# Performance work log

Measured on AMD Instinct MI355X. Metric: run time of the kernel, lower is better.

## Reference

```python
import jax, jax.numpy as jnp
import numpy as np

MARGIN = 1.0

def setup_inputs() -> dict:
    key = jax.random.key(0)
    B = 8192
    sim = jax.random.normal(key, (B, B), dtype=jnp.float32)
    return {"sim": sim}

def _half_loss(mat, offdiag):
    # mat: [B, B]; per-row pos = diagonal, neg = max over off-diag entries
    # satisfying neg + margin > pos. Rows with no valid neg are skipped (0).
    pos = jnp.diagonal(mat)                                   # [B]
    valid = offdiag & (mat + MARGIN > pos[:, None])           # [B, B]
    neg = jnp.max(jnp.where(valid, mat, -jnp.inf), axis=1)    # [B]
    has = jnp.any(valid, axis=1)                              # [B]
    neg_safe = jnp.where(has, neg, 0.0)
    pos_loss = jnp.clip(0.2 * pos * pos - 0.7 * pos + 0.5, 0.0)
    neg_loss = jnp.clip(0.9 * neg_safe * neg_safe - 0.4 * neg_safe + 0.03, 0.0)
    return jnp.sum(jnp.where(has, pos_loss + neg_loss, 0.0))

def reference(sim):
    B = sim.shape[0]
    offdiag = ~jnp.eye(B, dtype=bool)
    total = _half_loss(sim, offdiag) + _half_loss(sim.T, offdiag)
    return total / B
```

## Files before the change

### kernel.cpp

```cpp
#include <hip/hip_runtime.h>
#include <math.h>
#include <limits.h>

#define BN 8192
#define ROWS 32
#define TPB 256
#define NCB 8

__device__ __forceinline__ int map_f(float x) {
    int b = __float_as_int(x);
    return b >= 0 ? b : b ^ 0x7fffffff;
}
__device__ __forceinline__ float unmap_f(int m) {
    int b = m >= 0 ? m : m ^ 0x7fffffff;
    return __int_as_float(b);
}

__global__ __launch_bounds__(1024) void init_kernel(int* __restrict__ maxes) {
    int i = blockIdx.x * blockDim.x + threadIdx.x;
    if (i < 2 * BN) maxes[i] = INT_MIN;
}

__global__ __launch_bounds__(TPB) void max_kernel(const float* __restrict__ sim,
                                                  int* __restrict__ row_max_i,
                                                  int* __restrict__ col_max_i,
                                                  float* __restrict__ diag) {
    __shared__ float lds[ROWS * 4];
    const int t = threadIdx.x;
    const int bid = blockIdx.x;
    const int cb = bid & (NCB - 1);
    const int rbase = (bid >> 3) * ROWS;
    const int gf = cb * TPB + t;

    float4 cm = make_float4(-INFINITY, -INFINITY, -INFINITY, -INFINITY);

#pragma unroll 4
    for (int r = 0; r < ROWS; ++r) {
        const int gr = rbase + r;
        float4 v = ((const float4*)(sim + (size_t)gr * BN))[gf];
        if (gf == (gr >> 2)) {
            diag[gr] = ((float*)&v)[gr & 3];
            ((float*)&v)[gr & 3] = -INFINITY;
        }
        cm.x = fmaxf(cm.x, v.x);
        cm.y = fmaxf(cm.y, v.y);
        cm.z = fmaxf(cm.z, v.z);
        cm.w = fmaxf(cm.w, v.w);
        float m = fmaxf(fmaxf(v.x, v.y), fmaxf(v.z, v.w));
#pragma unroll
        for (int off = 32; off > 0; off >>= 1)
            m = fmaxf(m, __shfl_down(m, off, 64));
        if ((t & 63) == 0) lds[r * 4 + (t >> 6)] = m;
    }
    __syncthreads();
    if (t < ROWS) {
        float m = fmaxf(fmaxf(lds[t * 4 + 0], lds[t * 4 + 1]),
                        fmaxf(lds[t * 4 + 2], lds[t * 4 + 3]));
        atomicMax(&row_max_i[rbase + t], map_f(m));
    }
    const int c = 4 * gf;
    atomicMax(&col_max_i[c + 0], map_f(cm.x));
    atomicMax(&col_max_i[c + 1], map_f(cm.y));
    atomicMax(&col_max_i[c + 2], map_f(cm.z));
    atomicMax(&col_max_i[c + 3], map_f(cm.w));
}

__global__ __launch_bounds__(1024) void loss_kernel(const float* __restrict__ diag,
                                                    const int* __restrict__ row_max_i,
                                                    const int* __restrict__ col_max_i,
                                                    float* __restrict__ out) {
    __shared__ float lds[16];
    const int t = threadIdx.x;
    float sum = 0.0f;
#pragma unroll
    for (int k = 0; k < BN / 1024; ++k) {
        const int i = t + 1024 * k;
        const float pos = diag[i];
        const float pos_loss = fmaxf(0.2f * pos * pos - 0.7f * pos + 0.5f, 0.0f);

        const float rneg = unmap_f(row_max_i[i]);
        if (rneg + 1.0f > pos)
            sum += pos_loss + fmaxf(0.9f * rneg * rneg - 0.4f * rneg + 0.03f, 0.0f);

        const float cneg = unmap_f(col_max_i[i]);
        if (cneg + 1.0f > pos)
            sum += pos_loss + fmaxf(0.9f * cneg * cneg - 0.4f * cneg + 0.03f, 0.0f);
    }
#pragma unroll
    for (int off = 32; off > 0; off >>= 1)
        sum += __shfl_down(sum, off, 64);
    if ((t & 63) == 0) lds[t >> 6] = sum;
    __syncthreads();
    if (t == 0) {
        float total = 0.0f;
        for (int w = 0; w < 16; ++w) total += lds[w];
        out[0] = total / (float)BN;
    }
}

extern "C" void kernel_launch(void* const* d_in, const int* in_sizes, int n_in,
                              void* d_out, int out_size, void* d_ws, size_t ws_size,
                              hipStream_t stream) {
    const float* sim = (const float*)d_in[0];
    int*   row_max_i = (int*)d_ws;
    int*   col_max_i = (int*)((char*)d_ws + BN * sizeof(int));
    float* diag      = (float*)((char*)d_ws + 2 * BN * sizeof(int));
    float* out = (float*)d_out;

    init_kernel<<<(2 * BN) / 1024, 1024, 0, stream>>>(row_max_i);
    max_kernel<<<(BN / ROWS) * NCB, TPB, 0, stream>>>(sim, row_max_i, col_max_i, diag);
    loss_kernel<<<1, 1024, 0, stream>>>(diag, row_max_i, col_max_i, out);
}
```

Measured before the change: 377.4 us.

## Replace global atomic max reductions with partial buffers and a two-stage reduce

The max kernel now writes per-block row and column partial maxima to workspace buffers instead of issuing global atomicMax on integer-mapped floats. This also removes the init kernel. A new 64-block reduce kernel combines the partials and computes per-block loss sums, and a tiny final kernel sums those. This swaps atomic contention on 8192 column addresses for an extra 8 MB write and read of column partials.

```diff
diff --git a/kernel.cpp b/kernel.cpp
--- a/kernel.cpp
+++ b/kernel.cpp
@@ -1,35 +1,23 @@
 #include <hip/hip_runtime.h>
 #include <math.h>
-#include <limits.h>
 
 #define BN 8192
 #define ROWS 32
 #define TPB 256
 #define NCB 8
-
-__device__ __forceinline__ int map_f(float x) {
-    int b = __float_as_int(x);
-    return b >= 0 ? b : b ^ 0x7fffffff;
-}
-__device__ __forceinline__ float unmap_f(int m) {
-    int b = m >= 0 ? m : m ^ 0x7fffffff;
-    return __int_as_float(b);
-}
-
-__global__ __launch_bounds__(1024) void init_kernel(int* __restrict__ maxes) {
-    int i = blockIdx.x * blockDim.x + threadIdx.x;
-    if (i < 2 * BN) maxes[i] = INT_MIN;
-}
+#define NRG 256
+#define RBLK 64
 
 __global__ __launch_bounds__(TPB) void max_kernel(const float* __restrict__ sim,
-                                                  int* __restrict__ row_max_i,
-                                                  int* __restrict__ col_max_i,
+                                                  float* __restrict__ rowpart,
+                                                  float* __restrict__ colpart,
                                                   float* __restrict__ diag) {
     __shared__ float lds[ROWS * 4];
     const int t = threadIdx.x;
     const int bid = blockIdx.x;
     const int cb = bid & (NCB - 1);
-    const int rbase = (bid >> 3) * ROWS;
+    const int rg = bid >> 3;
+    const int rbase = rg * ROWS;
     const int gf = cb * TPB + t;
 
     float4 cm = make_float4(-INFINITY, -INFINITY, -INFINITY, -INFINITY);
@@ -56,58 +44,79 @@
     if (t < ROWS) {
         float m = fmaxf(fmaxf(lds[t * 4 + 0], lds[t * 4 + 1]),
                         fmaxf(lds[t * 4 + 2], lds[t * 4 + 3]));
-        atomicMax(&row_max_i[rbase + t], map_f(m));
+        rowpart[cb * BN + rbase + t] = m;
     }
-    const int c = 4 * gf;
-    atomicMax(&col_max_i[c + 0], map_f(cm.x));
-    atomicMax(&col_max_i[c + 1], map_f(cm.y));
-    atomicMax(&col_max_i[c + 2], map_f(cm.z));
-    atomicMax(&col_max_i[c + 3], map_f(cm.w));
+    ((float4*)(colpart + (size_t)rg * BN))[gf] = cm;
 }
 
-__global__ __launch_bounds__(1024) void loss_kernel(const float* __restrict__ diag,
-                                                    const int* __restrict__ row_max_i,
-                                                    const int* __restrict__ col_max_i,
-                                                    float* __restrict__ out) {
-    __shared__ float lds[16];
+__global__ __launch_bounds__(TPB) void reduce_loss(const float* __restrict__ rowpart,
+                                                   const float* __restrict__ colpart,
+                                                   const float* __restrict__ diag,
+                                                   float* __restrict__ block_sums) {
+    __shared__ float csh[TPB];
+    __shared__ float psum[4];
     const int t = threadIdx.x;
+    const int blk = blockIdx.x;
+    const int c = blk * 128 + (t & 127);
+    const int h = t >> 7;
+
+    float c0 = -INFINITY, c1 = -INFINITY, c2 = -INFINITY, c3 = -INFINITY;
+    for (int j = 0; j < 128; j += 4) {
+        const size_t base = (size_t)(h * 128 + j) * BN + c;
+        c0 = fmaxf(c0, colpart[base]);
+        c1 = fmaxf(c1, colpart[base + (size_t)BN]);
+        c2 = fmaxf(c2, colpart[base + (size_t)2 * BN]);
+        c3 = fmaxf(c3, colpart[base + (size_t)3 * BN]);
+    }
+    csh[t] = fmaxf(fmaxf(c0, c1), fmaxf(c2, c3));
+    __syncthreads();
+
     float sum = 0.0f;
+    if (t < 128) {
+        const int i = blk * 128 + t;
+        const float cneg = fmaxf(csh[t], csh[t + 128]);
+        float rneg = -INFINITY;
 #pragma unroll
-    for (int k = 0; k < BN / 1024; ++k) {
-        const int i = t + 1024 * k;
+        for (int cb = 0; cb < NCB; ++cb)
+            rneg = fmaxf(rneg, rowpart[cb * BN + i]);
         const float pos = diag[i];
         const float pos_loss = fmaxf(0.2f * pos * pos - 0.7f * pos + 0.5f, 0.0f);
-
-        const float rneg = unmap_f(row_max_i[i]);
         if (rneg + 1.0f > pos)
             sum += pos_loss + fmaxf(0.9f * rneg * rneg - 0.4f * rneg + 0.03f, 0.0f);
-
-        const float cneg = unmap_f(col_max_i[i]);
         if (cneg + 1.0f > pos)
             sum += pos_loss + fmaxf(0.9f * cneg * cneg - 0.4f * cneg + 0.03f, 0.0f);
     }
 #pragma unroll
     for (int off = 32; off > 0; off >>= 1)
         sum += __shfl_down(sum, off, 64);
-    if ((t & 63) == 0) lds[t >> 6] = sum;
+    if ((t & 63) == 0) psum[t >> 6] = sum;
     __syncthreads();
-    if (t == 0) {
-        float total = 0.0f;
-        for (int w = 0; w < 16; ++w) total += lds[w];
-        out[0] = total / (float)BN;
-    }
+    if (t == 0)
+        block_sums[blk] = (psum[0] + psum[1]) + (psum[2] + psum[3]);
+}
+
+__global__ __launch_bounds__(64) void final_kernel(const float* __restrict__ block_sums,
+                                                   float* __restrict__ out) {
+    const int t = threadIdx.x;
+    float s = block_sums[t];
+#pragma unroll
+    for (int off = 32; off > 0; off >>= 1)
+        s += __shfl_down(s, off, 64);
+    if (t == 0) out[0] = s / (float)BN;
 }
 
 extern "C" void kernel_launch(void* const* d_in, const int* in_sizes, int n_in,
                               void* d_out, int out_size, void* d_ws, size_t ws_size,
                               hipStream_t stream) {
     const float* sim = (const float*)d_in[0];
-    int*   row_max_i = (int*)d_ws;
-    int*   col_max_i = (int*)((char*)d_ws + BN * sizeof(int));
-    float* diag      = (float*)((char*)d_ws + 2 * BN * sizeof(int));
+    char* ws = (char*)d_ws;
+    float* colpart    = (float*)ws;
+    float* rowpart    = (float*)(ws + (size_t)NRG * BN * 4);
+    float* diag       = (float*)(ws + (size_t)(NRG + NCB) * BN * 4);
+    float* block_sums = (float*)(ws + (size_t)(NRG + NCB + 1) * BN * 4);
     float* out = (float*)d_out;
 
-    init_kernel<<<(2 * BN) / 1024, 1024, 0, stream>>>(row_max_i);
-    max_kernel<<<(BN / ROWS) * NCB, TPB, 0, stream>>>(sim, row_max_i, col_max_i, diag);
-    loss_kernel<<<1, 1024, 0, stream>>>(diag, row_max_i, col_max_i, out);
+    max_kernel<<<NRG * NCB, TPB, 0, stream>>>(sim, rowpart, colpart, diag);
+    reduce_loss<<<RBLK, TPB, 0, stream>>>(rowpart, colpart, diag, block_sums);
+    final_kernel<<<1, 64, 0, stream>>>(block_sums, out);
 }
```

Result: no change. 373.5 us (-1.0%).
